# Optimization experiments

Hardware: AMD Instinct MI355X
Metric: run time of the kernel (lower is better)

Reference implementation:

```python
import jax, jax.numpy as jnp
import numpy as np

BATCH, PATH_DIM = 2048, 2048
SIG_DIM = 14  # 2 + 2^2 + 2^3, depth-3 signature of a 2-channel path


def setup_inputs() -> dict:
    key = jax.random.key(0)
    ks = jax.random.split(key, 6)
    x = jax.random.normal(ks[0], (BATCH, 1, PATH_DIM), jnp.float32)
    w1 = jax.random.normal(ks[1], (8, 1), jnp.float32) * 0.5   # Augment conv1 (kernel=1)
    b1 = jax.random.normal(ks[2], (8,), jnp.float32) * 0.1
    w2 = jax.random.normal(ks[3], (2, 8), jnp.float32) * 0.3   # Augment conv2 (kernel=1)
    b2 = jax.random.normal(ks[4], (2,), jnp.float32) * 0.1
    w_out = jax.random.normal(ks[5], (SIG_DIM,), jnp.float32) * 0.2  # Linear(14,1,bias=False)
    return dict(x=x, w1=w1, b1=b1, w2=w2, b2=b2, w_out=w_out)


def _forward(x, w1, b1, w2, b2, w_out):
    # Augment: pointwise MLP (Conv1d, kernel_size=1), channels 1 -> 8 -> 2, ReLU between.
    h = jax.nn.relu(jnp.einsum('bcl,hc->bhl', x, w1) + b1[None, :, None])
    path = jnp.einsum('bhl,oh->bol', h, w2) + b2[None, :, None]   # (B, 2, L)
    p = jnp.transpose(path, (0, 2, 1))                            # (B, L, 2)
    dx = p[:, 1:, :] - p[:, :-1, :]                               # (B, N=L-1, 2) increments

    # Depth-3 signature of each linear segment with increment v:
    #   level1 = v, level2 = v^{\otimes 2}/2, level3 = v^{\otimes 3}/6.
    s1 = dx
    s2 = 0.5 * jnp.einsum('bni,bnj->bnij', dx, dx)
    s3 = (1.0 / 6.0) * jnp.einsum('bni,bnj,bnk->bnijk', dx, dx, dx)

    def chen(carry, seg):
        # Chen's identity: signature of concatenated path = carry \otimes seg.
        a1, a2, a3 = carry
        g1, g2, g3 = seg
        c1 = a1 + g1
        c2 = a2 + jnp.einsum('bi,bj->bij', a1, g1) + g2
        c3 = (a3 + jnp.einsum('bij,bk->bijk', a2, g1)
              + jnp.einsum('bi,bjk->bijk', a1, g2) + g3)
        B = c1.shape[0]
        flat = jnp.concatenate([c1, c2.reshape(B, 4), c3.reshape(B, 8)], axis=-1)  # (B, 14)
        return (c1, c2, c3), flat

    B = dx.shape[0]
    dt = dx.dtype
    init = (jnp.zeros((B, 2), dt), jnp.zeros((B, 2, 2), dt), jnp.zeros((B, 2, 2, 2), dt))
    segs = (jnp.swapaxes(s1, 0, 1), jnp.swapaxes(s2, 0, 1), jnp.swapaxes(s3, 0, 1))
    _, sigs = jax.lax.scan(chen, init, segs)          # (N, B, 14): sig of each prefix x[:,:,:i+2]
    # Tiny output projection Linear(14 -> 1, no bias), then stack/transpose -> (B, N)
    return jnp.einsum('nbs,s->bn', sigs, w_out)


def reference(x, w1, b1, w2, b2, w_out):
    return _forward(x, w1, b1, w2, b2, w_out)
```

## Files before the change

### kernel.cpp

```cpp
#include <hip/hip_runtime.h>

#define LPTS  2048
#define NSEG  2047
#define TPB   256
#define STEPS 8
#define NBATCH 2048
#define NWAVE (TPB / 64)

template <int CTRL, int RMASK, bool BC>
__device__ __forceinline__ float dpp_f(float s) {
    return __int_as_float(__builtin_amdgcn_update_dpp(
        0, __float_as_int(s), CTRL, RMASK, 0xF, BC));
}


__device__ __forceinline__ void chen_step7(float s[7], float vx, float vy,
                                           const float WO[14], float WO78,
                                           float WO1112) {
    const float qxx = 0.5f * vx * vx;
    const float qxy = 0.5f * vx * vy;
    const float qyy = 0.5f * vy * vy;
    const float wx = fmaf(vx, (1.0f / 3.0f), s[0]);
    const float wy = fmaf(vy, (1.0f / 3.0f), s[1]);
    const float tvxx = fmaf(WO[7], vy, WO[6] * vx);
    const float tvxy = fmaf(WO[9], vy, WO[8] * vx);
    const float tvyx = fmaf(WO[11], vy, WO[10] * vx);
    const float tvyy = fmaf(WO[13], vy, WO[12] * vx);
    const float tqx = fmaf(WO[9], qyy, fmaf(WO78, qxy, WO[6] * qxx));
    const float tqy = fmaf(WO[13], qyy, fmaf(WO1112, qxy, WO[10] * qxx));
    float z1 = fmaf(s[2], tvxx, s[6]);
    z1 = fmaf(s[4], tvyx, z1);
    z1 = fmaf(wx, tqx, z1);
    float z2 = fmaf(s[5], tvyy, s[3] * tvxy);
    z2 = fmaf(wy, tqy, z2);
    s[6] = z1 + z2;
    const float ux = fmaf(vx, 0.5f, s[0]);
    const float uy = fmaf(vy, 0.5f, s[1]);
    s[2] = fmaf(ux, vx, s[2]);
    s[3] = fmaf(ux, vy, s[3]);
    s[4] = fmaf(uy, vx, s[4]);
    s[5] = fmaf(uy, vy, s[5]);
    s[0] += vx;
    s[1] += vy;
}

__device__ __forceinline__ void chen_combine7(const float a[7], float b[7],
                                              const float WO[14]) {
    const float tvxx = fmaf(WO[7], b[1], WO[6] * b[0]);
    const float tvxy = fmaf(WO[9], b[1], WO[8] * b[0]);
    const float tvyx = fmaf(WO[11], b[1], WO[10] * b[0]);
    const float tvyy = fmaf(WO[13], b[1], WO[12] * b[0]);
    const float ubx = fmaf(WO[9], b[5], fmaf(WO[8], b[4], fmaf(WO[7], b[3], WO[6] * b[2])));
    const float uby = fmaf(WO[13], b[5], fmaf(WO[12], b[4], fmaf(WO[11], b[3], WO[10] * b[2])));
    float z1 = fmaf(a[2], tvxx, a[6] + b[6]);
    z1 = fmaf(a[4], tvyx, z1);
    z1 = fmaf(a[0], ubx, z1);
    float z2 = fmaf(a[5], tvyy, a[3] * tvxy);
    z2 = fmaf(a[1], uby, z2);
    const float cxx = a[2] + fmaf(a[0], b[0], b[2]);
    const float cxy = a[3] + fmaf(a[0], b[1], b[3]);
    const float cyx = a[4] + fmaf(a[1], b[0], b[4]);
    const float cyy = a[5] + fmaf(a[1], b[1], b[5]);
    b[0] = a[0] + b[0];
    b[1] = a[1] + b[1];
    b[2] = cxx;
    b[3] = cxy;
    b[4] = cyx;
    b[5] = cyy;
    b[6] = z1 + z2;
}

__device__ __forceinline__ void chen_combine6(const float a[6], float b[6]) {
    const float cxx = a[2] + fmaf(a[0], b[0], b[2]);
    const float cxy = a[3] + fmaf(a[0], b[1], b[3]);
    const float cyx = a[4] + fmaf(a[1], b[0], b[4]);
    const float cyy = a[5] + fmaf(a[1], b[1], b[5]);
    b[0] = a[0] + b[0];
    b[1] = a[1] + b[1];
    b[2] = cxx;
    b[3] = cxy;
    b[4] = cyx;
    b[5] = cyy;
}

__device__ __forceinline__ void augment(float x,
                                        const float W1[8], const float B1[8],
                                        const float W2x[8], const float W2y[8],
                                        float B2x, float B2y,
                                        float& px, float& py) {
    float ox = B2x, oy = B2y;
#pragma unroll
    for (int c = 0; c < 8; ++c) {
        float h = fmaxf(fmaf(W1[c], x, B1[c]), 0.0f);
        ox = fmaf(W2x[c], h, ox);
        oy = fmaf(W2y[c], h, oy);
    }
    px = ox;
    py = oy;
}

#define SCAN6_ROUND(CTRL, RMASK, BC)                                     \
    {                                                                    \
        float p[6];                                                      \
        _Pragma("unroll")                                                \
        for (int i = 0; i < 6; ++i) p[i] = dpp_f<CTRL, RMASK, BC>(s[i]); \
        chen_combine6(p, s);                                             \
    }

#define USCAN_ROUND(CTRL, RMASK, BC) u += dpp_f<CTRL, RMASK, BC>(u);

__global__ void sig_scan_kernel(
    const float* __restrict__ x, const float* __restrict__ w1,
    const float* __restrict__ b1, const float* __restrict__ w2,
    const float* __restrict__ b2, const float* __restrict__ wout,
    float* __restrict__ out) {
    __shared__ float wsum[NWAVE][8];

    const int t = threadIdx.x;
    const int lane = t & 63;
    const int wv = t >> 6;
    const int brow = blockIdx.x;
    const float* __restrict__ xrow = x + (size_t)brow * LPTS;

    float W1[8], B1[8], W2x[8], W2y[8];
#pragma unroll
    for (int c = 0; c < 8; ++c) {
        W1[c] = w1[c];
        B1[c] = b1[c];
        W2x[c] = w2[c];
        W2y[c] = w2[8 + c];
    }
    const float B2x = b2[0], B2y = b2[1];
    float WO[14];
#pragma unroll
    for (int i = 0; i < 14; ++i) WO[i] = wout[i];
    const float WO78 = WO[7] + WO[8];
    const float WO1112 = WO[11] + WO[12];

    const int n0 = t * STEPS;
    const float4 xa = *reinterpret_cast<const float4*>(xrow + n0);
    const float4 xb = *reinterpret_cast<const float4*>(xrow + n0 + 4);
    const int ib = (n0 + STEPS > LPTS - 1) ? (LPTS - 1) : (n0 + STEPS);
    const float x8 = xrow[ib];
    const float xv[STEPS + 1] = {xa.x, xa.y, xa.z, xa.w,
                                 xb.x, xb.y, xb.z, xb.w, x8};

    float vx[STEPS], vy[STEPS];
    float s[7] = {0, 0, 0, 0, 0, 0, 0};
    float ppx, ppy;
    augment(xv[0], W1, B1, W2x, W2y, B2x, B2y, ppx, ppy);
#pragma unroll
    for (int k = 0; k < STEPS; ++k) {
        float px, py;
        augment(xv[k + 1], W1, B1, W2x, W2y, B2x, B2y, px, py);
        vx[k] = px - ppx;
        vy[k] = py - ppy;
        ppx = px;
        ppy = py;
        chen_step7(s, vx[k], vy[k], WO, WO78, WO1112);
    }

    float sl[7];
#pragma unroll
    for (int i = 0; i < 7; ++i) sl[i] = s[i];

    SCAN6_ROUND(0x111, 0xF, true)
    SCAN6_ROUND(0x112, 0xF, true)
    SCAN6_ROUND(0x114, 0xF, true)
    SCAN6_ROUND(0x118, 0xF, true)
    SCAN6_ROUND(0x142, 0xA, false)
    SCAN6_ROUND(0x143, 0xC, false)

    float e[6];
#pragma unroll
    for (int i = 0; i < 6; ++i) e[i] = dpp_f<0x138, 0xF, true>(s[i]);

    float u;
    {
        const float tvxx = fmaf(WO[7], sl[1], WO[6] * sl[0]);
        const float tvxy = fmaf(WO[9], sl[1], WO[8] * sl[0]);
        const float tvyx = fmaf(WO[11], sl[1], WO[10] * sl[0]);
        const float tvyy = fmaf(WO[13], sl[1], WO[12] * sl[0]);
        const float ubx = fmaf(WO[9], sl[5], fmaf(WO[8], sl[4], fmaf(WO[7], sl[3], WO[6] * sl[2])));
        const float uby = fmaf(WO[13], sl[5], fmaf(WO[12], sl[4], fmaf(WO[11], sl[3], WO[10] * sl[2])));
        u = fmaf(e[2], tvxx, sl[6]);
        u = fmaf(e[3], tvxy, u);
        u = fmaf(e[4], tvyx, u);
        u = fmaf(e[5], tvyy, u);
        u = fmaf(e[0], ubx, u);
        u = fmaf(e[1], uby, u);
    }

    USCAN_ROUND(0x111, 0xF, true)
    USCAN_ROUND(0x112, 0xF, true)
    USCAN_ROUND(0x114, 0xF, true)
    USCAN_ROUND(0x118, 0xF, true)
    USCAN_ROUND(0x142, 0xA, false)
    USCAN_ROUND(0x143, 0xC, false)

    if (lane == 63) {
#pragma unroll
        for (int i = 0; i < 6; ++i) wsum[wv][i] = s[i];
        wsum[wv][6] = u;
    }
    __syncthreads();

    float a[7];
#pragma unroll
    for (int i = 0; i < 6; ++i) a[i] = e[i];
    a[6] = dpp_f<0x138, 0xF, true>(u);
    for (int w = wv - 1; w >= 0; --w) {
        float tw[7];
#pragma unroll
        for (int i = 0; i < 7; ++i) tw[i] = wsum[w][i];
        chen_combine7(tw, a, WO);
    }

    float* __restrict__ orow = out + (size_t)brow * NSEG;
#pragma unroll
    for (int k = 0; k < STEPS; ++k) {
        chen_step7(a, vx[k], vy[k], WO, WO78, WO1112);
        float o = a[6];
        o = fmaf(WO[0], a[0], o);
        o = fmaf(WO[1], a[1], o);
        o = fmaf(WO[2], a[2], o);
        o = fmaf(WO[3], a[3], o);
        o = fmaf(WO[4], a[4], o);
        o = fmaf(WO[5], a[5], o);
        const int n = n0 + k;
        if (n < NSEG) orow[n] = o;
    }
}

extern "C" void kernel_launch(void* const* d_in, const int* in_sizes, int n_in,
                              void* d_out, int out_size, void* d_ws, size_t ws_size,
                              hipStream_t stream) {
    const float* x  = (const float*)d_in[0];
    const float* w1 = (const float*)d_in[1];
    const float* b1 = (const float*)d_in[2];
    const float* w2 = (const float*)d_in[3];
    const float* b2 = (const float*)d_in[4];
    const float* wo = (const float*)d_in[5];
    float* out = (float*)d_out;
    sig_scan_kernel<<<NBATCH, TPB, 0, stream>>>(x, w1, b1, w2, b2, wo, out);
}
```

Before: 19.73 us.

## Reuse per-step level-3 contributions and linearize output projection around thread prefix

The first pass now returns and stores each step's projected level-3 increment (zeta), so it does not have to be recomputed later. The output pass stops re-running the full Chen step on the prefix-carried state. Instead it tracks only the local level-1/2 partial signature and evaluates the output as an affine function of it, with coefficients derived once from the thread's prefix. This cuts the per-output ALU work but keeps 8 more live registers per thread.

Result: no change. 19.70 us (-0.1%).

```diff
diff --git a/kernel.cpp b/kernel.cpp
--- a/kernel.cpp
+++ b/kernel.cpp
@@ -14,9 +14,9 @@
 }
 
 
-__device__ __forceinline__ void chen_step7(float s[7], float vx, float vy,
-                                           const float WO[14], float WO78,
-                                           float WO1112) {
+__device__ __forceinline__ float chen_step7z(float s[7], float vx, float vy,
+                                             const float WO[14], float WO78,
+                                             float WO1112) {
     const float qxx = 0.5f * vx * vx;
     const float qxy = 0.5f * vx * vy;
     const float qyy = 0.5f * vy * vy;
@@ -28,12 +28,13 @@
     const float tvyy = fmaf(WO[13], vy, WO[12] * vx);
     const float tqx = fmaf(WO[9], qyy, fmaf(WO78, qxy, WO[6] * qxx));
     const float tqy = fmaf(WO[13], qyy, fmaf(WO1112, qxy, WO[10] * qxx));
-    float z1 = fmaf(s[2], tvxx, s[6]);
+    float z1 = s[2] * tvxx;
     z1 = fmaf(s[4], tvyx, z1);
     z1 = fmaf(wx, tqx, z1);
     float z2 = fmaf(s[5], tvyy, s[3] * tvxy);
     z2 = fmaf(wy, tqy, z2);
-    s[6] = z1 + z2;
+    const float zeta = z1 + z2;
+    s[6] += zeta;
     const float ux = fmaf(vx, 0.5f, s[0]);
     const float uy = fmaf(vy, 0.5f, s[1]);
     s[2] = fmaf(ux, vx, s[2]);
@@ -42,6 +43,7 @@
     s[5] = fmaf(uy, vy, s[5]);
     s[0] += vx;
     s[1] += vy;
+    return zeta;
 }
 
 __device__ __forceinline__ void chen_combine7(const float a[7], float b[7],
@@ -145,7 +147,7 @@
     const float xv[STEPS + 1] = {xa.x, xa.y, xa.z, xa.w,
                                  xb.x, xb.y, xb.z, xb.w, x8};
 
-    float vx[STEPS], vy[STEPS];
+    float vx[STEPS], vy[STEPS], zeta[STEPS];
     float s[7] = {0, 0, 0, 0, 0, 0, 0};
     float ppx, ppy;
     augment(xv[0], W1, B1, W2x, W2y, B2x, B2y, ppx, ppy);
@@ -157,7 +159,7 @@
         vy[k] = py - ppy;
         ppx = px;
         ppy = py;
-        chen_step7(s, vx[k], vy[k], WO, WO78, WO1112);
+        zeta[k] = chen_step7z(s, vx[k], vy[k], WO, WO78, WO1112);
     }
 
     float sl[7];
@@ -216,17 +218,56 @@
         chen_combine7(tw, a, WO);
     }
 
+    float K0 = a[6];
+    K0 = fmaf(WO[0], a[0], K0);
+    K0 = fmaf(WO[1], a[1], K0);
+    K0 = fmaf(WO[2], a[2], K0);
+    K0 = fmaf(WO[3], a[3], K0);
+    K0 = fmaf(WO[4], a[4], K0);
+    K0 = fmaf(WO[5], a[5], K0);
+    float Kx = WO[0];
+    Kx = fmaf(WO[2], a[0], Kx);
+    Kx = fmaf(WO[4], a[1], Kx);
+    Kx = fmaf(WO[6], a[2], Kx);
+    Kx = fmaf(WO[8], a[3], Kx);
+    Kx = fmaf(WO[10], a[4], Kx);
+    Kx = fmaf(WO[12], a[5], Kx);
+    float Ky = WO[1];
+    Ky = fmaf(WO[3], a[0], Ky);
+    Ky = fmaf(WO[5], a[1], Ky);
+    Ky = fmaf(WO[7], a[2], Ky);
+    Ky = fmaf(WO[9], a[3], Ky);
+    Ky = fmaf(WO[11], a[4], Ky);
+    Ky = fmaf(WO[13], a[5], Ky);
+    const float Kxx = fmaf(WO[6], a[0], fmaf(WO[10], a[1], WO[2]));
+    const float Kxy = fmaf(WO[7], a[0], fmaf(WO[11], a[1], WO[3]));
+    const float Kyx = fmaf(WO[8], a[0], fmaf(WO[12], a[1], WO[4]));
+    const float Kyy = fmaf(WO[9], a[0], fmaf(WO[13], a[1], WO[5]));
+
+    float p1x = 0.0f, p1y = 0.0f;
+    float p2xx = 0.0f, p2xy = 0.0f, p2yx = 0.0f, p2yy = 0.0f;
+    float zp = 0.0f;
+
     float* __restrict__ orow = out + (size_t)brow * NSEG;
 #pragma unroll
     for (int k = 0; k < STEPS; ++k) {
-        chen_step7(a, vx[k], vy[k], WO, WO78, WO1112);
-        float o = a[6];
-        o = fmaf(WO[0], a[0], o);
-        o = fmaf(WO[1], a[1], o);
-        o = fmaf(WO[2], a[2], o);
-        o = fmaf(WO[3], a[3], o);
-        o = fmaf(WO[4], a[4], o);
-        o = fmaf(WO[5], a[5], o);
+        const float vxk = vx[k], vyk = vy[k];
+        const float ux = fmaf(vxk, 0.5f, p1x);
+        const float uy = fmaf(vyk, 0.5f, p1y);
+        p2xx = fmaf(ux, vxk, p2xx);
+        p2xy = fmaf(ux, vyk, p2xy);
+        p2yx = fmaf(uy, vxk, p2yx);
+        p2yy = fmaf(uy, vyk, p2yy);
+        p1x += vxk;
+        p1y += vyk;
+        zp += zeta[k];
+        float o = fmaf(Kx, p1x, K0);
+        o = fmaf(Ky, p1y, o);
+        o = fmaf(Kxx, p2xx, o);
+        o = fmaf(Kxy, p2xy, o);
+        o = fmaf(Kyx, p2yx, o);
+        o = fmaf(Kyy, p2yy, o);
+        o += zp;
         const int n = n0 + k;
         if (n < NSEG) orow[n] = o;
     }
```
